# Performance work log

Hardware: AMD Instinct MI355X
Metric: run time of the kernel (lower is better)

Reference implementation:

```python
import jax, jax.numpy as jnp
import numpy as np

B, H, K, L, V = 4096, 1024, 10, 64, 80  # batch, hidden, mixtures, char_len, vocab

def setup_inputs() -> dict:
    key = jax.random.key(0)
    k1, k2, k3, k4 = jax.random.split(key, 4)
    return {
        "x": jax.random.normal(k1, (B, H), dtype=jnp.float32),
        "chars": jax.random.normal(k2, (B, L, V), dtype=jnp.float32),
        "W": jax.random.normal(k3, (H, 3 * K), dtype=jnp.float32) * 0.02,
        "b": jax.random.normal(k4, (3 * K,), dtype=jnp.float32) * 0.02,
    }

def reference(x, chars, W, b):
    # Linear: [B, 3K]
    out = x @ W + b
    alpha_raw, beta_raw, kappa_raw = jnp.split(out, 3, axis=1)  # each [B, K]
    alpha = jnp.exp(alpha_raw)[:, :, None]            # [B, K, 1]
    beta = jnp.exp(beta_raw)[:, :, None]              # [B, K, 1]
    # kappa_prev is zero on first call -> kappa = exp(kappa_raw)
    kappa = jnp.exp(kappa_raw)[:, :, None]            # [B, K, 1]
    u = jnp.arange(L, dtype=jnp.float32)[None, None, :]  # [1, 1, L]
    phi = jnp.sum(alpha * jnp.exp(-beta * (kappa - u) ** 2), axis=1)  # [B, L]
    window = jnp.einsum('bl,blv->bv', phi, chars)     # [B, V]
    return window
```

## Files before the change

kernel.cpp:

```cpp
#include <hip/hip_runtime.h>
#include <math.h>

constexpr int Bn = 4096;
constexpr int Hn = 1024;
constexpr int Kn = 10;
constexpr int Ln = 64;
constexpr int Vn = 80;
constexpr int NJ = 3 * Kn;
constexpr int R  = 4;
constexpr int NT = 256;

__global__ __launch_bounds__(NT) void window_kernel(
    const float* __restrict__ x,
    const float* __restrict__ chars,
    const float* __restrict__ W,
    const float* __restrict__ bias,
    float* __restrict__ out)
{
    __shared__ float  xs[R * Hn];
    __shared__ float  part[R * 256];
    __shared__ float  abk[R * NJ];
    __shared__ float  phi_s[R * Ln];
    __shared__ float4 cpart[R * 12 * 20];

    const int t    = threadIdx.x;
    const int row0 = blockIdx.x * R;

    const float4* x4  = (const float4*)x;
    float4*       xs4 = (float4*)xs;
#pragma unroll
    for (int r = 0; r < R; ++r)
        xs4[r * (Hn / 4) + t] = x4[(size_t)(row0 + r) * (Hn / 4) + t];
    __syncthreads();

    const int j = t & 31;
    const int g = t >> 5;
    float acc0 = 0.f, acc1 = 0.f, acc2 = 0.f, acc3 = 0.f;
    if (j < NJ) {
        const float* Wp = W + j;
        const int h0 = g * 128;
#pragma unroll 4
        for (int ii = 0; ii < 128; ii += 4) {
            const int h  = h0 + ii;
            const int h4 = h >> 2;
            float4 xa = xs4[0 * (Hn / 4) + h4];
            float4 xb = xs4[1 * (Hn / 4) + h4];
            float4 xc = xs4[2 * (Hn / 4) + h4];
            float4 xd = xs4[3 * (Hn / 4) + h4];
            float w0 = Wp[(h + 0) * NJ];
            float w1 = Wp[(h + 1) * NJ];
            float w2 = Wp[(h + 2) * NJ];
            float w3 = Wp[(h + 3) * NJ];
            acc0 += w0 * xa.x + w1 * xa.y + w2 * xa.z + w3 * xa.w;
            acc1 += w0 * xb.x + w1 * xb.y + w2 * xb.z + w3 * xb.w;
            acc2 += w0 * xc.x + w1 * xc.y + w2 * xc.z + w3 * xc.w;
            acc3 += w0 * xd.x + w1 * xd.y + w2 * xd.z + w3 * xd.w;
        }
    }
    part[0 * 256 + g * 32 + j] = acc0;
    part[1 * 256 + g * 32 + j] = acc1;
    part[2 * 256 + g * 32 + j] = acc2;
    part[3 * 256 + g * 32 + j] = acc3;
    __syncthreads();

    if (t < R * NJ) {
        const int r = t / NJ, jj = t % NJ;
        float s = bias[jj];
#pragma unroll
        for (int gg = 0; gg < 8; ++gg) s += part[r * 256 + gg * 32 + jj];
        abk[r * NJ + jj] = __expf(s);
    }
    __syncthreads();

    {
        const int r = t >> 6, l = t & 63;
        const float lf = (float)l;
        const float* ab = abk + r * NJ;
        float ph = 0.f;
#pragma unroll
        for (int k = 0; k < Kn; ++k) {
            float a  = ab[k];
            float bt = ab[Kn + k];
            float kp = ab[2 * Kn + k];
            float d  = kp - lf;
            ph += a * __expf(-bt * d * d);
        }
        phi_s[r * Ln + l] = ph;
    }
    __syncthreads();

    const float4* c4 = (const float4*)chars;
    if (t < 240) {
        const int v4  = t % 20;
        const int g12 = t / 20;
        float4 s0 = make_float4(0.f, 0.f, 0.f, 0.f);
        float4 s1 = s0, s2 = s0, s3 = s0;
        for (int l = g12; l < Ln; l += 12) {
            const int off = l * 20 + v4;
            float4 cA = c4[(size_t)(row0 + 0) * 1280 + off];
            float4 cB = c4[(size_t)(row0 + 1) * 1280 + off];
            float4 cC = c4[(size_t)(row0 + 2) * 1280 + off];
            float4 cD = c4[(size_t)(row0 + 3) * 1280 + off];
            float p0 = phi_s[0 * Ln + l];
            float p1 = phi_s[1 * Ln + l];
            float p2 = phi_s[2 * Ln + l];
            float p3 = phi_s[3 * Ln + l];
            s0.x += p0 * cA.x; s0.y += p0 * cA.y; s0.z += p0 * cA.z; s0.w += p0 * cA.w;
            s1.x += p1 * cB.x; s1.y += p1 * cB.y; s1.z += p1 * cB.z; s1.w += p1 * cB.w;
            s2.x += p2 * cC.x; s2.y += p2 * cC.y; s2.z += p2 * cC.z; s2.w += p2 * cC.w;
            s3.x += p3 * cD.x; s3.y += p3 * cD.y; s3.z += p3 * cD.z; s3.w += p3 * cD.w;
        }
        cpart[(0 * 12 + g12) * 20 + v4] = s0;
        cpart[(1 * 12 + g12) * 20 + v4] = s1;
        cpart[(2 * 12 + g12) * 20 + v4] = s2;
        cpart[(3 * 12 + g12) * 20 + v4] = s3;
    }
    __syncthreads();

    if (t < 80) {
        const int r  = t / 20;
        const int vv = t % 20;
        float4 s = make_float4(0.f, 0.f, 0.f, 0.f);
#pragma unroll
        for (int gg = 0; gg < 12; ++gg) {
            float4 p = cpart[(r * 12 + gg) * 20 + vv];
            s.x += p.x; s.y += p.y; s.z += p.z; s.w += p.w;
        }
        ((float4*)out)[(size_t)(row0 + r) * 20 + vv] = s;
    }
}

extern "C" void kernel_launch(void* const* d_in, const int* in_sizes, int n_in,
                              void* d_out, int out_size, void* d_ws, size_t ws_size,
                              hipStream_t stream) {
    const float* x     = (const float*)d_in[0];
    const float* chars = (const float*)d_in[1];
    const float* W     = (const float*)d_in[2];
    const float* bias  = (const float*)d_in[3];
    float* out = (float*)d_out;

    window_kernel<<<Bn / R, NT, 0, stream>>>(x, chars, W, bias, out);
}
```

Baseline: 141.7 us.

## Process eight rows per 512-thread block and alias char partials onto x smem

```diff
diff --git a/kernel.cpp b/kernel.cpp
--- a/kernel.cpp
+++ b/kernel.cpp
@@ -7,67 +7,64 @@
 constexpr int Ln = 64;
 constexpr int Vn = 80;
 constexpr int NJ = 3 * Kn;
-constexpr int R  = 4;
-constexpr int NT = 256;
+constexpr int R  = 8;
+constexpr int NT = 512;
 
-__global__ __launch_bounds__(NT) void window_kernel(
+__global__ __launch_bounds__(NT) void window_fused(
     const float* __restrict__ x,
     const float* __restrict__ chars,
     const float* __restrict__ W,
     const float* __restrict__ bias,
     float* __restrict__ out)
 {
-    __shared__ float  xs[R * Hn];
-    __shared__ float  part[R * 256];
+    __shared__ float4 xs4[R * Hn / 4];
+    __shared__ float  part[R * 512];
     __shared__ float  abk[R * NJ];
     __shared__ float  phi_s[R * Ln];
-    __shared__ float4 cpart[R * 12 * 20];
 
     const int t    = threadIdx.x;
     const int row0 = blockIdx.x * R;
 
-    const float4* x4  = (const float4*)x;
-    float4*       xs4 = (float4*)xs;
+    const float4* xg4 = (const float4*)x + (size_t)row0 * (Hn / 4);
 #pragma unroll
-    for (int r = 0; r < R; ++r)
-        xs4[r * (Hn / 4) + t] = x4[(size_t)(row0 + r) * (Hn / 4) + t];
+    for (int i = 0; i < 4; ++i)
+        xs4[i * NT + t] = xg4[i * NT + t];
     __syncthreads();
 
-    const int j = t & 31;
-    const int g = t >> 5;
-    float acc0 = 0.f, acc1 = 0.f, acc2 = 0.f, acc3 = 0.f;
-    if (j < NJ) {
-        const float* Wp = W + j;
-        const int h0 = g * 128;
+    {
+        const int j = t & 31;
+        const int g = t >> 5;
+        float acc[R];
+#pragma unroll
+        for (int r = 0; r < R; ++r) acc[r] = 0.f;
+        if (j < NJ) {
+            const float* Wp = W + j;
+            const int h0 = g * 64;
 #pragma unroll 4
-        for (int ii = 0; ii < 128; ii += 4) {
-            const int h  = h0 + ii;
-            const int h4 = h >> 2;
-            float4 xa = xs4[0 * (Hn / 4) + h4];
-            float4 xb = xs4[1 * (Hn / 4) + h4];
-            float4 xc = xs4[2 * (Hn / 4) + h4];
-            float4 xd = xs4[3 * (Hn / 4) + h4];
-            float w0 = Wp[(h + 0) * NJ];
-            float w1 = Wp[(h + 1) * NJ];
-            float w2 = Wp[(h + 2) * NJ];
-            float w3 = Wp[(h + 3) * NJ];
-            acc0 += w0 * xa.x + w1 * xa.y + w2 * xa.z + w3 * xa.w;
-            acc1 += w0 * xb.x + w1 * xb.y + w2 * xb.z + w3 * xb.w;
-            acc2 += w0 * xc.x + w1 * xc.y + w2 * xc.z + w3 * xc.w;
-            acc3 += w0 * xd.x + w1 * xd.y + w2 * xd.z + w3 * xd.w;
+            for (int ii = 0; ii < 64; ii += 4) {
+                const int h  = h0 + ii;
+                const int h4 = h >> 2;
+                float w0 = Wp[(h + 0) * NJ];
+                float w1 = Wp[(h + 1) * NJ];
+                float w2 = Wp[(h + 2) * NJ];
+                float w3 = Wp[(h + 3) * NJ];
+#pragma unroll
+                for (int r = 0; r < R; ++r) {
+                    float4 v = xs4[r * 256 + h4];
+                    acc[r] += w0 * v.x + w1 * v.y + w2 * v.z + w3 * v.w;
+                }
+            }
         }
+#pragma unroll
+        for (int r = 0; r < R; ++r) part[r * 512 + g * 32 + j] = acc[r];
     }
-    part[0 * 256 + g * 32 + j] = acc0;
-    part[1 * 256 + g * 32 + j] = acc1;
-    part[2 * 256 + g * 32 + j] = acc2;
-    part[3 * 256 + g * 32 + j] = acc3;
     __syncthreads();
 
     if (t < R * NJ) {
         const int r = t / NJ, jj = t % NJ;
         float s = bias[jj];
 #pragma unroll
-        for (int gg = 0; gg < 8; ++gg) s += part[r * 256 + gg * 32 + jj];
+        for (int gg = 0; gg < 16; ++gg) s += part[r * 512 + gg * 32 + jj];
         abk[r * NJ + jj] = __expf(s);
     }
     __syncthreads();
@@ -89,41 +86,49 @@
     }
     __syncthreads();
 
+    float4* cpart = xs4;
     const float4* c4 = (const float4*)chars;
-    if (t < 240) {
-        const int v4  = t % 20;
-        const int g12 = t / 20;
+    const int half = t >> 8;
+    const int tt   = t & 255;
+    if (tt < 240) {
+        const int v4  = tt % 20;
+        const int g12 = tt / 20;
+        const int r0  = row0 + half * 4;
         float4 s0 = make_float4(0.f, 0.f, 0.f, 0.f);
         float4 s1 = s0, s2 = s0, s3 = s0;
         for (int l = g12; l < Ln; l += 12) {
             const int off = l * 20 + v4;
-            float4 cA = c4[(size_t)(row0 + 0) * 1280 + off];
-            float4 cB = c4[(size_t)(row0 + 1) * 1280 + off];
-            float4 cC = c4[(size_t)(row0 + 2) * 1280 + off];
-            float4 cD = c4[(size_t)(row0 + 3) * 1280 + off];
-            float p0 = phi_s[0 * Ln + l];
-            float p1 = phi_s[1 * Ln + l];
-            float p2 = phi_s[2 * Ln + l];
-            float p3 = phi_s[3 * Ln + l];
+            float4 cA = c4[(size_t)(r0 + 0) * 1280 + off];
+            float4 cB = c4[(size_t)(r0 + 1) * 1280 + off];
+            float4 cC = c4[(size_t)(r0 + 2) * 1280 + off];
+            float4 cD = c4[(size_t)(r0 + 3) * 1280 + off];
+            const float* ph = phi_s + half * 4 * Ln;
+            float p0 = ph[0 * Ln + l];
+            float p1 = ph[1 * Ln + l];
+            float p2 = ph[2 * Ln + l];
+            float p3 = ph[3 * Ln + l];
             s0.x += p0 * cA.x; s0.y += p0 * cA.y; s0.z += p0 * cA.z; s0.w += p0 * cA.w;
             s1.x += p1 * cB.x; s1.y += p1 * cB.y; s1.z += p1 * cB.z; s1.w += p1 * cB.w;
             s2.x += p2 * cC.x; s2.y += p2 * cC.y; s2.z += p2 * cC.z; s2.w += p2 * cC.w;
             s3.x += p3 * cD.x; s3.y += p3 * cD.y; s3.z += p3 * cD.z; s3.w += p3 * cD.w;
         }
-        cpart[(0 * 12 + g12) * 20 + v4] = s0;
-        cpart[(1 * 12 + g12) * 20 + v4] = s1;
-        cpart[(2 * 12 + g12) * 20 + v4] = s2;
-        cpart[(3 * 12 + g12) * 20 + v4] = s3;
+        float4* cp = cpart + half * 960;
+        cp[(0 * 12 + g12) * 20 + v4] = s0;
+        cp[(1 * 12 + g12) * 20 + v4] = s1;
+        cp[(2 * 12 + g12) * 20 + v4] = s2;
+        cp[(3 * 12 + g12) * 20 + v4] = s3;
     }
     __syncthreads();
 
-    if (t < 80) {
+    if (t < R * 20) {
         const int r  = t / 20;
         const int vv = t % 20;
+        const float4* cp = cpart + (r / 4) * 960;
+        const int rl = r & 3;
         float4 s = make_float4(0.f, 0.f, 0.f, 0.f);
 #pragma unroll
         for (int gg = 0; gg < 12; ++gg) {
-            float4 p = cpart[(r * 12 + gg) * 20 + vv];
+            float4 p = cp[(rl * 12 + gg) * 20 + vv];
             s.x += p.x; s.y += p.y; s.z += p.z; s.w += p.w;
         }
         ((float4*)out)[(size_t)(row0 + r) * 20 + vv] = s;
@@ -139,5 +144,5 @@
     const float* bias  = (const float*)d_in[3];
     float* out = (float*)d_out;
 
-    window_kernel<<<Bn / R, NT, 0, stream>>>(x, chars, W, bias, out);
+    window_fused<<<Bn / R, NT, 0, stream>>>(x, chars, W, bias, out);
 }
```

Measured after the change: 153.3 us. 1.08x slower.
